# Performance work log

Measured on AMD Instinct MI355X. Metric: run time of the kernel, lower is better.

Reference implementation:

```python
import jax, jax.numpy as jnp
import numpy as np

WS = 14            # window side (14x14 patches)
DIM = 768          # model dim (ViT-Base)
H = 12             # heads
HD = DIM // H      # head dim = 64
B = 128            # batch
N = WS * WS + 1    # 197 tokens (patches + CLS)
NRD = (2 * WS - 1) ** 2 + 3  # num_relative_distance = 732


def _rel_index():
    # Faithful replication of the torch buffer construction.
    coords = np.stack(np.meshgrid(np.arange(WS), np.arange(WS), indexing='ij'))  # [2,WS,WS]
    flat = coords.reshape(2, -1)                                   # [2, WS*WS]
    rel = flat[:, :, None] - flat[:, None, :]                      # [2, P, P]
    rel = rel.transpose(1, 2, 0).astype(np.int64)                  # [P, P, 2]
    rel[:, :, 0] += WS - 1
    rel[:, :, 1] += WS - 1
    rel[:, :, 0] *= 2 * WS - 1
    idx = np.zeros((N, N), dtype=np.int64)
    idx[1:, 1:] = rel.sum(-1)
    idx[0, :] = NRD - 3
    idx[:, 0] = NRD - 2
    idx[0, 0] = NRD - 1
    return jnp.asarray(idx, dtype=jnp.int32)


def setup_inputs() -> dict:
    key = jax.random.key(0)
    ks = jax.random.split(key, 5)
    return {
        'x': jax.random.normal(ks[0], (B, N, DIM), dtype=jnp.float32),
        'qkv_w': jax.random.normal(ks[1], (3 * DIM, DIM), dtype=jnp.float32) * 0.02,
        'q_bias': jnp.zeros((DIM,), jnp.float32),
        'v_bias': jnp.zeros((DIM,), jnp.float32),
        'rpb_table': jax.random.normal(ks[2], (NRD, H), dtype=jnp.float32) * 0.02,
        'proj_w': jax.random.normal(ks[3], (DIM, DIM), dtype=jnp.float32) * 0.02,
        'proj_b': jnp.zeros((DIM,), jnp.float32),
        'rel_idx': _rel_index(),
    }


def reference(x, qkv_w, q_bias, v_bias, rpb_table, proj_w, proj_b, rel_idx):
    Bv, Nv, C = x.shape
    scale = HD ** -0.5
    # qkv_bias = cat(q_bias, zeros, v_bias); eval mode so dropout is identity
    bias = jnp.concatenate([q_bias, jnp.zeros_like(v_bias), v_bias])
    qkv = x @ qkv_w.T + bias                                   # [B,N,3*DIM]
    qkv = qkv.reshape(Bv, Nv, 3, H, HD).transpose(2, 0, 3, 1, 4)
    q, k, v = qkv[0] * scale, qkv[1], qkv[2]                   # [B,H,N,HD]
    attn = jnp.einsum('bhqd,bhkd->bhqk', q, k)                 # [B,H,N,N]
    rpb = rpb_table[rel_idx]                                   # gather -> [N,N,H]
    attn = attn + rpb.transpose(2, 0, 1)[None]                 # + [1,H,N,N]
    attn = jax.nn.softmax(attn, axis=-1)
    out = jnp.einsum('bhqk,bhkd->bhqd', attn, v)               # [B,H,N,HD]
    out = out.transpose(0, 2, 1, 3).reshape(Bv, Nv, H * HD)
    return out @ proj_w.T + proj_b
```

## Files before the change

kernel.cpp:

```cpp
#include <hip/hip_runtime.h>
#include <hip/hip_bf16.h>
#include <cstdint>

#define BATCH 128
#define NTOK  197
#define NHEAD 12

typedef __attribute__((ext_vector_type(8))) __bf16 bf16x8;
typedef __attribute__((ext_vector_type(4))) float f32x4;
typedef __attribute__((ext_vector_type(4))) unsigned short ushort4v;

#define KSTR 72

__device__ __forceinline__ unsigned short f2bf(float f) {
    union { float f; unsigned int u; } v; v.f = f;
    unsigned int r = (v.u + 0x7FFFu + ((v.u >> 16) & 1u)) >> 16;
    return (unsigned short)r;
}

__device__ __forceinline__ void async_cp16(const void* gsrc, void* lds_dst) {
    __builtin_amdgcn_global_load_lds(
        (const __attribute__((address_space(1))) unsigned int*)((uintptr_t)gsrc),
        (__attribute__((address_space(3))) unsigned int*)((uintptr_t)lds_dst),
        16, 0, 0);
}

__global__ void bias_tiles(const float* __restrict__ rpb,
                           const int* __restrict__ rel_idx,
                           float* __restrict__ BT) {
    int idx = blockIdx.x * 256 + threadIdx.x;
    int r    = idx & 3;
    int j    = (idx >> 2) & 3;
    int l16  = (idx >> 4) & 15;
    int quad = (idx >> 8) & 3;
    int kt   = (idx >> 10) & 3;
    int qt   = (idx >> 12) & 15;
    int h    = idx >> 16;
    int qn = qt * 16 + quad * 4 + r; if (qn > 196) qn = 196;
    int kn = kt * 64 + j * 16 + l16;
    float v = 0.f;
    if (kn < NTOK) v = rpb[rel_idx[qn * NTOK + kn] * NHEAD + h];
    BT[idx] = v;
}

__global__ __launch_bounds__(256) void cvt_bf16(const float4* __restrict__ src,
                                                ushort4v* __restrict__ dst, int n4) {
    int i = blockIdx.x * 256 + threadIdx.x;
    if (i >= n4) return;
    float4 f = src[i];
    ushort4v o;
    o.x = f2bf(f.x); o.y = f2bf(f.y); o.z = f2bf(f.z); o.w = f2bf(f.w);
    dst[i] = o;
}

__global__ __launch_bounds__(256) void zero_buf(uint4* __restrict__ p, int n) {
    int i = blockIdx.x * 256 + threadIdx.x;
    if (i < n) p[i] = (uint4){0u, 0u, 0u, 0u};
}

template <int EPI>
__global__ __launch_bounds__(256) void gemm_mfma(
    const unsigned short* __restrict__ A,
    const unsigned short* __restrict__ W,
    const float* __restrict__ bias1, const float* __restrict__ bias2,
    unsigned short* __restrict__ oq, unsigned short* __restrict__ ok,
    unsigned short* __restrict__ ov,
    float* __restrict__ outf,
    int Mc) {
    __shared__ unsigned short As[128 * 32];
    __shared__ unsigned short Bs[128 * 32];

    const int t    = threadIdx.x;
    const int lane = t & 63;
    const int wave = t >> 6;
    const int wm   = wave >> 1;
    const int wn   = wave & 1;
    const int quad = lane >> 4;
    const int l16  = lane & 15;

    const int gx  = gridDim.x;
    const int nwg = gx * gridDim.y;
    const int orig = blockIdx.y * gx + blockIdx.x;
    const int q8 = nwg >> 3, r8 = nwg & 7;
    const int xcd = orig & 7, rest = orig >> 3;
    const int wg = (xcd < r8 ? xcd * (q8 + 1) : r8 * (q8 + 1) + (xcd - r8) * q8) + rest;
    const int m0 = (wg / gx) * 128;
    const int n0 = (wg % gx) * 128;

    const int srow = lane >> 2;
    const int scol = ((lane & 3) ^ (srow & 3)) * 8;
    int ar0 = m0 + wave * 32 + srow;      if (ar0 >= Mc) ar0 = Mc - 1;
    int ar1 = m0 + wave * 32 + 16 + srow; if (ar1 >= Mc) ar1 = Mc - 1;
    const unsigned short* Ag0 = A + (size_t)ar0 * 768 + scol;
    const unsigned short* Ag1 = A + (size_t)ar1 * 768 + scol;
    const unsigned short* Wg0 = W + (size_t)(n0 + wave * 32 + srow) * 768 + scol;
    const unsigned short* Wg1 = Wg0 + (size_t)16 * 768;
    unsigned short* Ad0 = As + (wave * 32) * 32;
    unsigned short* Ad1 = As + (wave * 32 + 16) * 32;
    unsigned short* Bd0 = Bs + (wave * 32) * 32;
    unsigned short* Bd1 = Bs + (wave * 32 + 16) * 32;

    const unsigned short* Afp = As + (wm * 64 + l16) * 32 + ((quad ^ (l16 & 3)) * 8);
    const unsigned short* Bfp = Bs + (wn * 64 + l16) * 32 + ((quad ^ (l16 & 3)) * 8);

    f32x4 acc[4][4] = {};

    for (int k0 = 0; k0 < 768; k0 += 32) {
        __syncthreads();
        async_cp16(Ag0 + k0, Ad0);
        async_cp16(Ag1 + k0, Ad1);
        async_cp16(Wg0 + k0, Bd0);
        async_cp16(Wg1 + k0, Bd1);
        __syncthreads();
        bf16x8 af[4], bfr[4];
#pragma unroll
        for (int i = 0; i < 4; i++) af[i]  = *(const bf16x8*)(Afp + i * 16 * 32);
#pragma unroll
        for (int j = 0; j < 4; j++) bfr[j] = *(const bf16x8*)(Bfp + j * 16 * 32);
#pragma unroll
        for (int i = 0; i < 4; i++)
#pragma unroll
            for (int j = 0; j < 4; j++)
                acc[i][j] = __builtin_amdgcn_mfma_f32_16x16x32_bf16(
                    af[i], bfr[j], acc[i][j], 0, 0, 0);
    }

    if (EPI == 0) {
        const int part = n0 / 768;
        const int nb0  = n0 - part * 768;
        if (part < 2) {
            const float scale = (part == 0) ? 0.125f : 1.f;
            unsigned short* dst = (part == 0) ? oq : ok;
#pragma unroll
            for (int j = 0; j < 4; j++) {
                const int nnb = nb0 + wn * 64 + j * 16;
                const int h   = nnb >> 6;
                const int d   = (nnb & 63) + l16;
                const float bb = (part == 0) ? bias1[nnb + l16] : 0.f;
#pragma unroll
                for (int i = 0; i < 4; i++) {
                    const int mb = m0 + wm * 64 + i * 16 + quad * 4;
#pragma unroll
                    for (int r = 0; r < 4; r++) {
                        const int m = mb + r;
                        if (m < Mc) {
                            const int bi  = m / NTOK;
                            const int tok = m - bi * NTOK;
                            dst[(((size_t)bi * NHEAD + h) * NTOK + tok) * 64 + d] =
                                f2bf((acc[i][j][r] + bb) * scale);
                        }
                    }
                }
            }
        } else {
#pragma unroll
            for (int j = 0; j < 4; j++) {
                const int nnb = nb0 + wn * 64 + j * 16;
                const int h   = nnb >> 6;
                const int d   = (nnb & 63) + l16;
                const float bb = bias2[nnb + l16];
#pragma unroll
                for (int i = 0; i < 4; i++) {
                    const int mb = m0 + wm * 64 + i * 16 + quad * 4;
#pragma unroll
                    for (int r = 0; r < 4; r++) {
                        const int m = mb + r;
                        if (m < Mc) {
                            const int bi  = m / NTOK;
                            const int tok = m - bi * NTOK;
                            ov[(((size_t)bi * NHEAD + h) * 64 + d) * 256 + tok] =
                                f2bf(acc[i][j][r] + bb);
                        }
                    }
                }
            }
        }
    } else {
#pragma unroll
        for (int j = 0; j < 4; j++) {
            const int col = n0 + wn * 64 + j * 16 + l16;
            const float bb = bias1[col];
#pragma unroll
            for (int i = 0; i < 4; i++) {
                const int mb = m0 + wm * 64 + i * 16 + quad * 4;
#pragma unroll
                for (int r = 0; r < 4; r++) {
                    const int m = mb + r;
                    if (m < Mc) outf[(size_t)m * 768 + col] = acc[i][j][r] + bb;
                }
            }
        }
    }
}

__global__ __launch_bounds__(256, 2) void attn_mfma(
    const unsigned short* __restrict__ Q, const unsigned short* __restrict__ K,
    const unsigned short* __restrict__ VT, const float* __restrict__ BT,
    unsigned short* __restrict__ AO) {
    __shared__ unsigned short Ks[64 * 64];
    __shared__ unsigned short Vt[64 * 64];
    __shared__ unsigned short Ps[4][64 * KSTR];

    const int t    = threadIdx.x;
    const int lane = t & 63;
    const int wave = t >> 6;
    const int quad = lane >> 4;
    const int l16  = lane & 15;
    const int bh   = blockIdx.x;
    const int b    = bh / NHEAD;
    const int h    = bh - b * NHEAD;

    const unsigned short* qb  = Q  + (size_t)bh * NTOK * 64;
    const unsigned short* kb  = K  + (size_t)bh * NTOK * 64;
    const unsigned short* vtg = VT + (size_t)bh * 64 * 256;

    bf16x8 qf[4][2];
#pragma unroll
    for (int i = 0; i < 4; i++) {
        int tok = wave * 64 + i * 16 + l16; if (tok > 196) tok = 196;
#pragma unroll
        for (int ks = 0; ks < 2; ks++)
            qf[i][ks] = *(const bf16x8*)&qb[(size_t)tok * 64 + ks * 32 + quad * 8];
    }

    f32x4 O[4][4] = {};
    float lsum[4][4] = {};

    for (int kt = 0; kt < 4; kt++) {
        __syncthreads();
        {
            const int rsub = wave * 8 + (lane >> 3);
            const int chk  = ((lane & 7) ^ (lane >> 3)) * 8;
            int gk0 = kt * 64 + rsub;      if (gk0 > 196) gk0 = 196;
            int gk1 = kt * 64 + 32 + rsub; if (gk1 > 196) gk1 = 196;
            async_cp16(kb + (size_t)gk0 * 64 + chk, Ks + wave * 512);
            async_cp16(kb + (size_t)gk1 * 64 + chk, Ks + 2048 + wave * 512);
            async_cp16(vtg + (size_t)rsub * 256 + kt * 64 + chk, Vt + wave * 512);
            async_cp16(vtg + (size_t)(32 + rsub) * 256 + kt * 64 + chk,
                       Vt + 2048 + wave * 512);
        }

        f32x4 acc[4][4];
#pragma unroll
        for (int i = 0; i < 4; i++) {
            const float4* bp = (const float4*)&BT[
                (((((size_t)h * 16 + (wave * 4 + i)) * 4 + kt) * 4 + quad) * 16 + l16) * 16];
#pragma unroll
            for (int j = 0; j < 4; j++) {
                float4 f = bp[j];
                acc[i][j] = (f32x4){f.x, f.y, f.z, f.w};
            }
        }

        asm volatile("s_waitcnt vmcnt(0)" ::: "memory");
        __builtin_amdgcn_s_barrier();

#pragma unroll
        for (int ks = 0; ks < 2; ks++) {
            bf16x8 kf[4];
#pragma unroll
            for (int j = 0; j < 4; j++)
                kf[j] = *(const bf16x8*)&Ks[(j * 16 + l16) * 64 +
                                            (((ks * 4 + quad) ^ (l16 & 7)) * 8)];
            __builtin_amdgcn_s_setprio(1);
#pragma unroll
            for (int i = 0; i < 4; i++)
#pragma unroll
                for (int j = 0; j < 4; j++)
                    acc[i][j] = __builtin_amdgcn_mfma_f32_16x16x32_bf16(
                        qf[i][ks], kf[j], acc[i][j], 0, 0, 0);
            __builtin_amdgcn_s_setprio(0);
        }

#pragma unroll
        for (int j = 0; j < 4; j++) {
            const int kn = kt * 64 + j * 16 + l16;
            const bool kval = (kn < NTOK);
#pragma unroll
            for (int i = 0; i < 4; i++)
#pragma unroll
                for (int r = 0; r < 4; r++) {
                    float p = kval ? __expf(fminf(acc[i][j][r], 30.f)) : 0.f;
                    lsum[i][r] += p;
                    Ps[wave][(i * 16 + quad * 4 + r) * KSTR + j * 16 + l16] = f2bf(p);
                }
        }

#pragma unroll
        for (int ks = 0; ks < 2; ks++) {
            bf16x8 vf[4], pf[4];
#pragma unroll
            for (int jd = 0; jd < 4; jd++)
                vf[jd] = *(const bf16x8*)&Vt[(jd * 16 + l16) * 64 +
                                             (((ks * 4 + quad) ^ (l16 & 7)) * 8)];
#pragma unroll
            for (int i = 0; i < 4; i++)
                pf[i] = *(const bf16x8*)&Ps[wave][(i * 16 + l16) * KSTR + ks * 32 + quad * 8];
            __builtin_amdgcn_s_setprio(1);
#pragma unroll
            for (int i = 0; i < 4; i++)
#pragma unroll
                for (int jd = 0; jd < 4; jd++)
                    O[i][jd] = __builtin_amdgcn_mfma_f32_16x16x32_bf16(
                        pf[i], vf[jd], O[i][jd], 0, 0, 0);
            __builtin_amdgcn_s_setprio(0);
        }
    }

#pragma unroll
    for (int i = 0; i < 4; i++)
#pragma unroll
        for (int r = 0; r < 4; r++) {
            float l = lsum[i][r];
            l += __shfl_xor(l, 1); l += __shfl_xor(l, 2);
            l += __shfl_xor(l, 4); l += __shfl_xor(l, 8);
            lsum[i][r] = 1.f / l;
        }
#pragma unroll
    for (int i = 0; i < 4; i++) {
        const int tb = wave * 64 + i * 16 + quad * 4;
#pragma unroll
        for (int r = 0; r < 4; r++) {
            const int tok = tb + r;
            if (tok < NTOK) {
                const float rl = lsum[i][r];
#pragma unroll
                for (int jd = 0; jd < 4; jd++)
                    AO[((size_t)b * NTOK + tok) * 768 + h * 64 + jd * 16 + l16] =
                        f2bf(O[i][jd][r] * rl);
            }
        }
    }
}

extern "C" void kernel_launch(void* const* d_in, const int* in_sizes, int n_in,
                              void* d_out, int out_size, void* d_ws, size_t ws_size,
                              hipStream_t stream) {
    const float* x      = (const float*)d_in[0];
    const float* qkv_w  = (const float*)d_in[1];
    const float* q_bias = (const float*)d_in[2];
    const float* v_bias = (const float*)d_in[3];
    const float* rpb    = (const float*)d_in[4];
    const float* proj_w = (const float*)d_in[5];
    const float* proj_b = (const float*)d_in[6];
    const int*   rel_idx = (const int*)d_in[7];
    float* out = (float*)d_out;

    const size_t EB   = 151296;
    const size_t VTE  = 196608;
    const size_t NBT  = 786432;
    const size_t NX   = (size_t)BATCH * NTOK * 768;
    const size_t NWQ  = (size_t)2304 * 768;
    const size_t NWP  = (size_t)768 * 768;

    const size_t fixed_bytes = NBT * 4 + (NX + NWQ + NWP) * 2;
    const size_t per_b = 2ull * (3 * EB + VTE);
    int Bc = BATCH;
    while (Bc > 1 && fixed_bytes + (size_t)Bc * per_b > ws_size) Bc >>= 1;
    if (fixed_bytes + (size_t)Bc * per_b > ws_size) return;
    const int nc = BATCH / Bc;
    const int Mc = Bc * NTOK;
    const int Gy = (Mc + 127) / 128;

    float* BT             = (float*)d_ws;
    unsigned short* xbf   = (unsigned short*)(BT + NBT);
    unsigned short* wqkv  = xbf + NX;
    unsigned short* wproj = wqkv + NWQ;
    unsigned short* q     = wproj + NWP;
    unsigned short* k     = q + (size_t)Bc * EB;
    unsigned short* vt    = k + (size_t)Bc * EB;
    unsigned short* aobf  = vt + (size_t)Bc * VTE;

    const int nz = Bc * 24576;
    zero_buf<<<(nz + 255) / 256, 256, 0, stream>>>((uint4*)vt, nz);
    bias_tiles<<<(int)(NBT / 256), 256, 0, stream>>>(rpb, rel_idx, BT);
    cvt_bf16<<<(int)((NX / 4 + 255) / 256), 256, 0, stream>>>(
        (const float4*)x, (ushort4v*)xbf, (int)(NX / 4));
    cvt_bf16<<<(int)((NWQ / 4 + 255) / 256), 256, 0, stream>>>(
        (const float4*)qkv_w, (ushort4v*)wqkv, (int)(NWQ / 4));
    cvt_bf16<<<(int)((NWP / 4 + 255) / 256), 256, 0, stream>>>(
        (const float4*)proj_w, (ushort4v*)wproj, (int)(NWP / 4));

    for (int c = 0; c < nc; c++) {
        gemm_mfma<0><<<dim3(2304 / 128, Gy), 256, 0, stream>>>(
            xbf + (size_t)c * Mc * 768, wqkv, q_bias, v_bias, q, k, vt, nullptr, Mc);
        attn_mfma<<<Bc * NHEAD, 256, 0, stream>>>(q, k, vt, BT, aobf);
        gemm_mfma<1><<<dim3(768 / 128, Gy), 256, 0, stream>>>(
            aobf, wproj, proj_b, nullptr, nullptr, nullptr, nullptr,
            out + (size_t)c * Mc * 768, Mc);
    }
}
```

Measured before the change: 460.3 us.

## Double-buffer K/V tiles in attention, remap GEMM LDS layout, simplify epilogue indexing

The attention kernel now keeps two LDS buffers for K and V and prefetches the next key tile while the current one is computed, so the global-load wait overlaps with MFMA work. Key masking moves into the precomputed bias tiles (-1e30 for padded keys), which drops the per-element validity select before exp. The GEMM changes its LDS staging layout to pack two rows per 64-element line with a new swizzle, and the epilogue replaces per-element division by NTOK with an incremental batch/token computation. In exchange, LDS use per attention block rises, which may lower occupancy at two blocks per CU, and the new GEMM swizzle could change bank-conflict behaviour.

```diff
diff --git a/kernel.cpp b/kernel.cpp
--- a/kernel.cpp
+++ b/kernel.cpp
@@ -38,7 +38,7 @@
     int h    = idx >> 16;
     int qn = qt * 16 + quad * 4 + r; if (qn > 196) qn = 196;
     int kn = kt * 64 + j * 16 + l16;
-    float v = 0.f;
+    float v = -1e30f;
     if (kn < NTOK) v = rpb[rel_idx[qn * NTOK + kn] * NHEAD + h];
     BT[idx] = v;
 }
@@ -87,36 +87,37 @@
     const int m0 = (wg / gx) * 128;
     const int n0 = (wg % gx) * 128;
 
-    const int srow = lane >> 2;
-    const int scol = ((lane & 3) ^ (srow & 3)) * 8;
-    int ar0 = m0 + wave * 32 + srow;      if (ar0 >= Mc) ar0 = Mc - 1;
-    int ar1 = m0 + wave * 32 + 16 + srow; if (ar1 >= Mc) ar1 = Mc - 1;
-    const unsigned short* Ag0 = A + (size_t)ar0 * 768 + scol;
-    const unsigned short* Ag1 = A + (size_t)ar1 * 768 + scol;
-    const unsigned short* Wg0 = W + (size_t)(n0 + wave * 32 + srow) * 768 + scol;
-    const unsigned short* Wg1 = Wg0 + (size_t)16 * 768;
-    unsigned short* Ad0 = As + (wave * 32) * 32;
-    unsigned short* Ad1 = As + (wave * 32 + 16) * 32;
-    unsigned short* Bd0 = Bs + (wave * 32) * 32;
-    unsigned short* Bd1 = Bs + (wave * 32 + 16) * 32;
-
-    const unsigned short* Afp = As + (wm * 64 + l16) * 32 + ((quad ^ (l16 & 3)) * 8);
-    const unsigned short* Bfp = Bs + (wn * 64 + l16) * 32 + ((quad ^ (l16 & 3)) * 8);
+    const int grow = wave * 16 + ((lane >> 3) << 1) + ((lane >> 2) & 1);
+    const int kcol = (((lane & 3) ^ ((lane >> 3) & 3)) << 3);
+    const unsigned short* Ag[2];
+    const unsigned short* Bg[2];
+#pragma unroll
+    for (int i = 0; i < 2; i++) {
+        int ra = m0 + i * 64 + grow; if (ra >= Mc) ra = Mc - 1;
+        Ag[i] = A + (size_t)ra * 768 + kcol;
+        Bg[i] = W + (size_t)(n0 + i * 64 + grow) * 768 + kcol;
+    }
+
+    const int l2  = l16 >> 1;
+    const int par = l16 & 1;
+    const int xr  = l2 & 3;
+    const unsigned short* Afp = As + (wm * 32 + l2) * 64 + par * 32 + ((quad ^ xr) << 3);
+    const unsigned short* Bfp = Bs + (wn * 32 + l2) * 64 + par * 32 + ((quad ^ xr) << 3);
 
     f32x4 acc[4][4] = {};
 
     for (int k0 = 0; k0 < 768; k0 += 32) {
         __syncthreads();
-        async_cp16(Ag0 + k0, Ad0);
-        async_cp16(Ag1 + k0, Ad1);
-        async_cp16(Wg0 + k0, Bd0);
-        async_cp16(Wg1 + k0, Bd1);
+        async_cp16(Ag[0] + k0, As + wave * 512);
+        async_cp16(Ag[1] + k0, As + 2048 + wave * 512);
+        async_cp16(Bg[0] + k0, Bs + wave * 512);
+        async_cp16(Bg[1] + k0, Bs + 2048 + wave * 512);
         __syncthreads();
         bf16x8 af[4], bfr[4];
 #pragma unroll
-        for (int i = 0; i < 4; i++) af[i]  = *(const bf16x8*)(Afp + i * 16 * 32);
-#pragma unroll
-        for (int j = 0; j < 4; j++) bfr[j] = *(const bf16x8*)(Bfp + j * 16 * 32);
+        for (int i = 0; i < 4; i++) af[i]  = *(const bf16x8*)(Afp + i * 512);
+#pragma unroll
+        for (int j = 0; j < 4; j++) bfr[j] = *(const bf16x8*)(Bfp + j * 512);
 #pragma unroll
         for (int i = 0; i < 4; i++)
 #pragma unroll
@@ -128,6 +129,8 @@
     if (EPI == 0) {
         const int part = n0 / 768;
         const int nb0  = n0 - part * 768;
+        const int bi0  = m0 / NTOK;
+        const int tk0  = m0 - bi0 * NTOK;
         if (part < 2) {
             const float scale = (part == 0) ? 0.125f : 1.f;
             unsigned short* dst = (part == 0) ? oq : ok;
@@ -139,13 +142,14 @@
                 const float bb = (part == 0) ? bias1[nnb + l16] : 0.f;
 #pragma unroll
                 for (int i = 0; i < 4; i++) {
-                    const int mb = m0 + wm * 64 + i * 16 + quad * 4;
+                    const int off = wm * 64 + i * 16 + quad * 4;
 #pragma unroll
                     for (int r = 0; r < 4; r++) {
-                        const int m = mb + r;
+                        const int m = m0 + off + r;
                         if (m < Mc) {
-                            const int bi  = m / NTOK;
-                            const int tok = m - bi * NTOK;
+                            int tok = tk0 + off + r;
+                            int bi  = bi0;
+                            if (tok >= NTOK) { tok -= NTOK; bi++; }
                             dst[(((size_t)bi * NHEAD + h) * NTOK + tok) * 64 + d] =
                                 f2bf((acc[i][j][r] + bb) * scale);
                         }
@@ -161,13 +165,14 @@
                 const float bb = bias2[nnb + l16];
 #pragma unroll
                 for (int i = 0; i < 4; i++) {
-                    const int mb = m0 + wm * 64 + i * 16 + quad * 4;
+                    const int off = wm * 64 + i * 16 + quad * 4;
 #pragma unroll
                     for (int r = 0; r < 4; r++) {
-                        const int m = mb + r;
+                        const int m = m0 + off + r;
                         if (m < Mc) {
-                            const int bi  = m / NTOK;
-                            const int tok = m - bi * NTOK;
+                            int tok = tk0 + off + r;
+                            int bi  = bi0;
+                            if (tok >= NTOK) { tok -= NTOK; bi++; }
                             ov[(((size_t)bi * NHEAD + h) * 64 + d) * 256 + tok] =
                                 f2bf(acc[i][j][r] + bb);
                         }
@@ -197,8 +202,8 @@
     const unsigned short* __restrict__ Q, const unsigned short* __restrict__ K,
     const unsigned short* __restrict__ VT, const float* __restrict__ BT,
     unsigned short* __restrict__ AO) {
-    __shared__ unsigned short Ks[64 * 64];
-    __shared__ unsigned short Vt[64 * 64];
+    __shared__ unsigned short Ks[2][64 * 64];
+    __shared__ unsigned short Vt[2][64 * 64];
     __shared__ unsigned short Ps[4][64 * KSTR];
 
     const int t    = threadIdx.x;
@@ -214,6 +219,19 @@
     const unsigned short* kb  = K  + (size_t)bh * NTOK * 64;
     const unsigned short* vtg = VT + (size_t)bh * 64 * 256;
 
+    const int rsub = wave * 8 + (lane >> 3);
+    const int chk  = ((lane & 7) ^ (lane >> 3)) * 8;
+
+    auto stage = [&](int buf, int kt) {
+        int gk0 = kt * 64 + rsub;      if (gk0 > 196) gk0 = 196;
+        int gk1 = kt * 64 + 32 + rsub; if (gk1 > 196) gk1 = 196;
+        async_cp16(kb + (size_t)gk0 * 64 + chk, Ks[buf] + wave * 512);
+        async_cp16(kb + (size_t)gk1 * 64 + chk, Ks[buf] + 2048 + wave * 512);
+        async_cp16(vtg + (size_t)rsub * 256 + kt * 64 + chk, Vt[buf] + wave * 512);
+        async_cp16(vtg + (size_t)(32 + rsub) * 256 + kt * 64 + chk,
+                   Vt[buf] + 2048 + wave * 512);
+    };
+
     bf16x8 qf[4][2];
 #pragma unroll
     for (int i = 0; i < 4; i++) {
@@ -226,19 +244,12 @@
     f32x4 O[4][4] = {};
     float lsum[4][4] = {};
 
+    stage(0, 0);
+    asm volatile("s_waitcnt vmcnt(0)" ::: "memory");
+    __builtin_amdgcn_s_barrier();
+
     for (int kt = 0; kt < 4; kt++) {
-        __syncthreads();
-        {
-            const int rsub = wave * 8 + (lane >> 3);
-            const int chk  = ((lane & 7) ^ (lane >> 3)) * 8;
-            int gk0 = kt * 64 + rsub;      if (gk0 > 196) gk0 = 196;
-            int gk1 = kt * 64 + 32 + rsub; if (gk1 > 196) gk1 = 196;
-            async_cp16(kb + (size_t)gk0 * 64 + chk, Ks + wave * 512);
-            async_cp16(kb + (size_t)gk1 * 64 + chk, Ks + 2048 + wave * 512);
-            async_cp16(vtg + (size_t)rsub * 256 + kt * 64 + chk, Vt + wave * 512);
-            async_cp16(vtg + (size_t)(32 + rsub) * 256 + kt * 64 + chk,
-                       Vt + 2048 + wave * 512);
-        }
+        const int buf = kt & 1;
 
         f32x4 acc[4][4];
 #pragma unroll
@@ -252,16 +263,15 @@
             }
         }
 
-        asm volatile("s_waitcnt vmcnt(0)" ::: "memory");
-        __builtin_amdgcn_s_barrier();
+        if (kt < 3) stage(buf ^ 1, kt + 1);
 
 #pragma unroll
         for (int ks = 0; ks < 2; ks++) {
             bf16x8 kf[4];
 #pragma unroll
             for (int j = 0; j < 4; j++)
-                kf[j] = *(const bf16x8*)&Ks[(j * 16 + l16) * 64 +
-                                            (((ks * 4 + quad) ^ (l16 & 7)) * 8)];
+                kf[j] = *(const bf16x8*)&Ks[buf][(j * 16 + l16) * 64 +
+                                               (((ks * 4 + quad) ^ (l16 & 7)) * 8)];
             __builtin_amdgcn_s_setprio(1);
 #pragma unroll
             for (int i = 0; i < 4; i++)
@@ -273,26 +283,23 @@
         }
 
 #pragma unroll
-        for (int j = 0; j < 4; j++) {
-            const int kn = kt * 64 + j * 16 + l16;
-            const bool kval = (kn < NTOK);
+        for (int j = 0; j < 4; j++)
 #pragma unroll
             for (int i = 0; i < 4; i++)
 #pragma unroll
                 for (int r = 0; r < 4; r++) {
-                    float p = kval ? __expf(fminf(acc[i][j][r], 30.f)) : 0.f;
+                    float p = __expf(fminf(acc[i][j][r], 30.f));
                     lsum[i][r] += p;
                     Ps[wave][(i * 16 + quad * 4 + r) * KSTR + j * 16 + l16] = f2bf(p);
                 }
-        }
 
 #pragma unroll
         for (int ks = 0; ks < 2; ks++) {
             bf16x8 vf[4], pf[4];
 #pragma unroll
             for (int jd = 0; jd < 4; jd++)
-                vf[jd] = *(const bf16x8*)&Vt[(jd * 16 + l16) * 64 +
-                                             (((ks * 4 + quad) ^ (l16 & 7)) * 8)];
+                vf[jd] = *(const bf16x8*)&Vt[buf][(jd * 16 + l16) * 64 +
+                                                 (((ks * 4 + quad) ^ (l16 & 7)) * 8)];
 #pragma unroll
             for (int i = 0; i < 4; i++)
                 pf[i] = *(const bf16x8*)&Ps[wave][(i * 16 + l16) * KSTR + ks * 32 + quad * 8];
@@ -305,6 +312,9 @@
                         pf[i], vf[jd], O[i][jd], 0, 0, 0);
             __builtin_amdgcn_s_setprio(0);
         }
+
+        asm volatile("s_waitcnt vmcnt(0)" ::: "memory");
+        __builtin_amdgcn_s_barrier();
     }
 
 #pragma unroll
```

Result: no change. 456.3 us (-0.9%).
